# Kernel tuning notes

Measured on AMD Instinct MI355X. Metric: run time of the kernel, lower is better.

The kernel has to match this reference:

```python
import jax, jax.numpy as jnp
import numpy as np

DIM = 512
MAX_LEN = 2048
SHARED = 128
EXPAND = 2 * DIM  # expansion_factor * dim
PROJ = 2 * EXPAND + SHARED
EPS = 1e-6
BATCH = 8


def _rope(x):
    # x: [n, d]; rotates last dim (split-half RoPE) with position along axis 0
    n, d = x.shape
    half = d // 2
    freq = jnp.arange(half, dtype=x.dtype) / float(half)
    inv_freq = 10000.0 ** (-freq)
    sinusoid = jnp.arange(n, dtype=x.dtype)[:, None] * inv_freq[None, :]  # [n, half]
    sin, cos = jnp.sin(sinusoid), jnp.cos(sinusoid)
    x1, x2 = x[:, :half], x[:, half:]
    return jnp.concatenate([x1 * cos - x2 * sin, x2 * cos + x1 * sin], axis=-1)


def _toeplitz_rope(n, a, b):
    # a, b: [max_len]; tile to [n, max_len], rope over positions, then outer product
    ar = _rope(jnp.tile(a[None, :], (n, 1)))
    br = _rope(jnp.tile(b[None, :], (n, 1)))
    return jnp.einsum('mk,nk->mn', ar, br)  # [n, n]


def setup_inputs() -> dict:
    key = jax.random.key(0)
    ks = jax.random.split(key, 8)
    std = 0.02
    return {
        'x': jax.random.normal(ks[0], (BATCH, MAX_LEN, DIM), jnp.float32),
        'W1': std * jax.random.normal(ks[1], (DIM, PROJ), jnp.float32),
        'b1': jnp.zeros((PROJ,), jnp.float32),
        'W2': std * jax.random.normal(ks[2], (EXPAND, DIM), jnp.float32),
        'b2': jnp.zeros((DIM,), jnp.float32),
        'rope_a': std * jax.random.normal(ks[3], (MAX_LEN,), jnp.float32),
        'rope_b': std * jax.random.normal(ks[4], (MAX_LEN,), jnp.float32),
        'gamma': std * jax.random.normal(ks[5], (2, SHARED), jnp.float32),
        'beta': jnp.zeros((2, SHARED), jnp.float32),
        'norm_scale': jnp.asarray(1.0, jnp.float32),
    }


def reference(x, W1, b1, W2, b2, rope_a, rope_b, gamma, beta, norm_scale):
    shortcut = x
    # ScaledNorm: x * rsqrt(mean(x^2)) * scale
    ms = jnp.mean(jnp.square(x), axis=-1, keepdims=True)
    xn = x * jax.lax.rsqrt(ms + EPS) * norm_scale
    # proj1 with swish activation
    uv = jax.nn.swish(xn @ W1 + b1)  # [b, n, PROJ]
    u = uv[..., :EXPAND]
    v = uv[..., EXPAND:2 * EXPAND]
    base = uv[..., 2 * EXPAND:]  # [b, n, SHARED]
    qk_base = base[:, :, None, :] * gamma + beta  # [b, n, 2, SHARED]
    q, k = qk_base[:, :, 0, :], qk_base[:, :, 1, :]
    qk = jnp.einsum('bnd,bmd->bnm', q, k) / float(MAX_LEN)
    qk = qk + _toeplitz_rope(MAX_LEN, rope_a, rope_b)
    kernel = jnp.square(jax.nn.relu(qk))  # sqrrelu
    o = u * jnp.einsum('bnm,bme->bne', kernel, v)
    return o @ W2 + b2 + shortcut
```

## Files before the change

kernel.cpp:

```cpp
#include <hip/hip_runtime.h>
#include <math.h>

#define SEQ    2048
#define DIMM   512
#define SH     128
#define EXP    1024
#define PROJ_  2176
#define NBATCH 8
#define ROWS   16384

#define KER_SCALE     16384.0f
#define KER_SCALE_INV (1.0f / 16384.0f)
#define QK_INV        (1.0f / (4096.0f * 2048.0f))
#define W8            64.0f
#define INV4096       (1.0f / 4096.0f)

typedef __attribute__((ext_vector_type(4))) float floatx4;
typedef __attribute__((ext_vector_type(8))) int   int8v;

__device__ __forceinline__ unsigned short f2bf(float f) {
  union { float f; unsigned int u; } v; v.f = f;
  unsigned int r = (v.u + 0x7fffu + ((v.u >> 16) & 1u)) >> 16;
  return (unsigned short)r;
}
__device__ __forceinline__ float bf2f(unsigned short h) {
  union { unsigned int u; float f; } v; v.u = ((unsigned int)h) << 16;
  return v.f;
}
__device__ __forceinline__ unsigned char f2fp8(float f) {
  return (unsigned char)(__builtin_amdgcn_cvt_pk_fp8_f32(f, 0.0f, 0, false) & 0xffu);
}
__device__ __forceinline__ unsigned int pk4fp8(float a, float b, float c, float d) {
  unsigned int w = __builtin_amdgcn_cvt_pk_fp8_f32(a, b, 0, false);
  return __builtin_amdgcn_cvt_pk_fp8_f32(c, d, w, true);
}
__device__ __forceinline__ float fp82f(unsigned char b) {
  int e = (b >> 3) & 15, m = b & 7;
  float v = ldexpf((float)(e ? (8 + m) : m), (e ? e : 1) - 10);
  return (b & 0x80) ? -v : v;
}

__device__ __forceinline__ void async16(const void* g, void* l) {
  __builtin_amdgcn_global_load_lds(
      (const __attribute__((address_space(1))) void*)g,
      (__attribute__((address_space(3))) void*)l, 16, 0, 0);
}

__device__ __forceinline__ void transpose_tile_fp8(const float* __restrict__ in,
                                                   unsigned char* __restrict__ out,
                                                   int R, int C, int bx, int by, float* tile) {
  int tx = threadIdx.x & 31, ty = threadIdx.x >> 5;
  int c0 = bx * 32, r0 = by * 32;
  #pragma unroll
  for (int j = 0; j < 32; j += 8)
    tile[(ty + j) * 33 + tx] = in[(long)(r0 + ty + j) * C + c0 + tx];
  __syncthreads();
  #pragma unroll
  for (int j = 0; j < 32; j += 8)
    out[(long)(c0 + ty + j) * R + r0 + tx] = f2fp8(tile[tx * 33 + ty + j] * W8);
}

__global__ void prep_kernel(const float* __restrict__ x, const float* __restrict__ ns,
                            unsigned char* __restrict__ xq,
                            const float* __restrict__ W1, unsigned char* __restrict__ w1q,
                            const float* __restrict__ W2, unsigned char* __restrict__ w2q,
                            const float* __restrict__ ra, const float* __restrict__ rb,
                            float* __restrict__ tpl) {
  __shared__ float sh[33 * 32];
  const int b = blockIdx.x, tid = threadIdx.x;
  if (b < 4096) {
    int wave = tid >> 6, lane = tid & 63;
    long row = (long)b * 4 + wave;
    const float4* xr = (const float4*)(x + row * DIMM);
    float4 v0 = xr[lane], v1 = xr[lane + 64];
    float ss = v0.x*v0.x + v0.y*v0.y + v0.z*v0.z + v0.w*v0.w
             + v1.x*v1.x + v1.y*v1.y + v1.z*v1.z + v1.w*v1.w;
    #pragma unroll
    for (int o = 32; o > 0; o >>= 1) ss += __shfl_xor(ss, o);
    float sc = rsqrtf(ss * (1.0f / DIMM) + 1e-6f) * ns[0] * W8;
    uint2 pk;
    pk.x = pk4fp8(v0.x*sc, v0.y*sc, v0.z*sc, v0.w*sc);
    pk.y = pk4fp8(v1.x*sc, v1.y*sc, v1.z*sc, v1.w*sc);
    ((uint2*)(xq + row * DIMM))[lane] = pk;
  } else if (b < 4096 + 4095) {
    const int d = (b - 4096) - 2047;
    float sum = 0.0f;
    for (int k = tid; k < 1024; k += 256) {
      float a1 = ra[k], a2 = ra[k + 1024];
      float b1v = rb[k], b2v = rb[k + 1024];
      float p = a1 * b1v + a2 * b2v;
      float q = a1 * b2v - a2 * b1v;
      float th = exp2f((float)k * (-13.287712379549449f / 1024.0f));
      float ang = (float)d * th;
      sum += p * cosf(ang) + q * sinf(ang);
    }
    #pragma unroll
    for (int o = 32; o > 0; o >>= 1) sum += __shfl_xor(sum, o);
    int wave = tid >> 6, lane = tid & 63;
    if (lane == 0) sh[wave] = sum;
    __syncthreads();
    if (tid == 0) tpl[b - 4096] = sh[0] + sh[1] + sh[2] + sh[3];
  } else if (b < 9279) {
    int t = b - 8191;
    transpose_tile_fp8(W1, w1q, DIMM, PROJ_, t % 68, t / 68, sh);
  } else {
    int t = b - 9279;
    transpose_tile_fp8(W2, w2q, EXP, DIMM, t % 16, t / 16, sh);
  }
}

__device__ __forceinline__ void mfma_core_mx(const unsigned char* __restrict__ A,
                                             const unsigned char* __restrict__ B,
                                             int K, long rowBase, long colBase,
                                             unsigned char* smem, floatx4 acc[4][4]) {
  unsigned char* As = smem;
  unsigned char* Bs = smem + 128 * 128;
  const int tid  = threadIdx.x;
  const int wave = tid >> 6;
  const int lane = tid & 63;
  const int wr   = (wave >> 1) * 64;
  const int wc   = (wave & 1) * 64;
  const int r_l  = lane >> 3;
  const int c8   = lane & 7;
  const int fm   = lane & 15;
  const int fq   = lane >> 4;

  floatx4 z = {0.0f, 0.0f, 0.0f, 0.0f};
  #pragma unroll
  for (int mi = 0; mi < 4; ++mi)
    #pragma unroll
    for (int ni = 0; ni < 4; ++ni) acc[mi][ni] = z;

  union U8 { uint4 q[2]; int8v v; };

  for (int k0 = 0; k0 < K; k0 += 128) {
    __syncthreads();
    #pragma unroll
    for (int j = 0; j < 4; ++j) {
      int row = j * 32 + wave * 8 + r_l;
      int g = c8 ^ (row & 7);
      async16(A + (rowBase + row) * (long)K + k0 + g * 16, As + (j * 32 + wave * 8) * 128);
      async16(B + (colBase + row) * (long)K + k0 + g * 16, Bs + (j * 32 + wave * 8) * 128);
    }
    __syncthreads();
    int8v av[4], bv[4];
    #pragma unroll
    for (int mi = 0; mi < 4; ++mi) {
      int row = wr + mi * 16 + fm;
      int s0 = (2 * fq) ^ (row & 7);
      U8 u;
      u.q[0] = *(const uint4*)(As + row * 128 + s0 * 16);
      u.q[1] = *(const uint4*)(As + row * 128 + (s0 ^ 1) * 16);
      av[mi] = u.v;
    }
    #pragma unroll
    for (int ni = 0; ni < 4; ++ni) {
      int row = wc + ni * 16 + fm;
      int s0 = (2 * fq) ^ (row & 7);
      U8 u;
      u.q[0] = *(const uint4*)(Bs + row * 128 + s0 * 16);
      u.q[1] = *(const uint4*)(Bs + row * 128 + (s0 ^ 1) * 16);
      bv[ni] = u.v;
    }
    #pragma unroll
    for (int mi = 0; mi < 4; ++mi)
      #pragma unroll
      for (int ni = 0; ni < 4; ++ni)
        acc[mi][ni] = __builtin_amdgcn_mfma_scale_f32_16x16x128_f8f6f4(
            av[mi], bv[ni], acc[mi][ni], 0, 0, 0, 0x7F7F7F7F, 0, 0x7F7F7F7F);
  }
}

#define EPILOGUE_VARS                                         \
  const int lane = threadIdx.x & 63, wave = threadIdx.x >> 6; \
  const int wr = (wave >> 1) * 64, wc = (wave & 1) * 64;      \
  const int fr = (lane >> 4) * 4, fc = lane & 15;

__global__ void __launch_bounds__(256)
gemm_uv(const unsigned char* __restrict__ xq,
        const unsigned char* __restrict__ w1q,
        const float* __restrict__ b1,
        const float* __restrict__ gamma,
        const float* __restrict__ beta,
        unsigned char* __restrict__ uq,
        unsigned char* __restrict__ vT,
        unsigned char* __restrict__ qq,
        unsigned char* __restrict__ kq) {
  __shared__ __align__(16) unsigned short smem[17408];
  floatx4 acc[4][4];
  long rowBase = (long)blockIdx.x * 128;
  long colBase = (long)blockIdx.y * 128;
  mfma_core_mx(xq, w1q, DIMM, rowBase, colBase, (unsigned char*)smem, acc);
  EPILOGUE_VARS

  if (blockIdx.y < 8) {
    #pragma unroll
    for (int mi = 0; mi < 4; ++mi)
    #pragma unroll
    for (int ni = 0; ni < 4; ++ni)
    #pragma unroll
    for (int i = 0; i < 4; ++i) {
      long row = rowBase + wr + mi * 16 + fr + i;
      long col = colBase + wc + ni * 16 + fc;
      float t = acc[mi][ni][i] * INV4096 + b1[col];
      uq[row * EXP + col] = f2fp8(t / (1.0f + __expf(-t)) * W8);
    }
  } else if (blockIdx.y < 16) {
    __syncthreads();
    #pragma unroll
    for (int mi = 0; mi < 4; ++mi)
    #pragma unroll
    for (int ni = 0; ni < 4; ++ni)
    #pragma unroll
    for (int i = 0; i < 4; ++i) {
      int rl = wr + mi * 16 + fr + i;
      int cl = wc + ni * 16 + fc;
      long col = colBase + cl;
      float t = acc[mi][ni][i] * INV4096 + b1[col];
      smem[cl * 136 + rl] = f2bf(t / (1.0f + __expf(-t)));
    }
    __syncthreads();
    long b_   = rowBase >> 11;
    long nblk = rowBase & 2047;
    long e0   = colBase - EXP;
    #pragma unroll
    for (int rep = 0; rep < 8; ++rep) {
      int cl = rep * 16 + (threadIdx.x >> 4);
      int n0 = (threadIdx.x & 15) * 8;
      const unsigned short* src = smem + cl * 136 + n0;
      uint2 pk;
      pk.x = pk4fp8(bf2f(src[0]), bf2f(src[1]), bf2f(src[2]), bf2f(src[3]));
      pk.y = pk4fp8(bf2f(src[4]), bf2f(src[5]), bf2f(src[6]), bf2f(src[7]));
      *(uint2*)(vT + (b_ * EXP + e0 + cl) * (long)SEQ + nblk + n0) = pk;
    }
  } else {
    #pragma unroll
    for (int mi = 0; mi < 4; ++mi)
    #pragma unroll
    for (int ni = 0; ni < 4; ++ni)
    #pragma unroll
    for (int i = 0; i < 4; ++i) {
      long row = rowBase + wr + mi * 16 + fr + i;
      long col = colBase + wc + ni * 16 + fc;
      float t = acc[mi][ni][i] * INV4096 + b1[col];
      float s = t / (1.0f + __expf(-t));
      int dd = (int)(col - 2 * EXP);
      qq[row * SH + dd] = f2fp8((s * gamma[dd] + beta[dd]) * W8);
      kq[row * SH + dd] = f2fp8((s * gamma[SH + dd] + beta[SH + dd]) * W8);
    }
  }
}

__global__ void __launch_bounds__(256)
gemm_qk(const unsigned char* __restrict__ kq,
        const unsigned char* __restrict__ qq,
        const float* __restrict__ tpl,
        unsigned char* __restrict__ ker) {
  __shared__ __align__(16) unsigned char smem8[32768];
  floatx4 acc[4][4];
  int L = blockIdx.x;
  long b = L & 7;
  int w = L >> 3;
  long mBase = (long)(w & 15) * 128;
  long nBase = (long)(w >> 4) * 128;
  mfma_core_mx(kq + b * SEQ * SH, qq + b * SEQ * SH, SH, mBase, nBase, smem8, acc);
  unsigned char* kerb = ker + b * (long)SEQ * SEQ;
  EPILOGUE_VARS
  (void)fr;
  __syncthreads();
  #pragma unroll
  for (int mi = 0; mi < 4; ++mi)
  #pragma unroll
  for (int ni = 0; ni < 4; ++ni) {
    int m_loc0 = wr + mi * 16 + (lane >> 4) * 4;
    int n_loc  = wc + ni * 16 + fc;
    long n = nBase + n_loc;
    long m0 = mBase + m_loc0;
    float v[4];
    #pragma unroll
    for (int i = 0; i < 4; ++i) {
      float val = acc[mi][ni][i] * QK_INV + tpl[n - (m0 + i) + 2047];
      float r = fmaxf(val, 0.0f);
      v[i] = fminf(r * r * KER_SCALE, 440.0f);
    }
    *(unsigned int*)(smem8 + n_loc * 136 + m_loc0) = pk4fp8(v[0], v[1], v[2], v[3]);
  }
  __syncthreads();
  #pragma unroll
  for (int rep = 0; rep < 4; ++rep) {
    int n_loc = rep * 32 + (threadIdx.x >> 3);
    int m_seg = (threadIdx.x & 7) * 16;
    uint4 v16 = *(const uint4*)(smem8 + n_loc * 136 + m_seg);
    *(uint4*)(kerb + (nBase + n_loc) * (long)SEQ + mBase + m_seg) = v16;
  }
}

__global__ void __launch_bounds__(256)
gemm_pv(const unsigned char* __restrict__ ker,
        const unsigned char* __restrict__ vT,
        const unsigned char* __restrict__ uq,
        unsigned char* __restrict__ obq) {
  __shared__ __align__(16) unsigned char smem8[32768];
  floatx4 acc[4][4];
  int L = blockIdx.x;
  long b = L & 7;
  int w = L >> 3;
  long eBase = (long)(w & 7) * 128;
  long nBase = (long)(w >> 3) * 128;
  mfma_core_mx(vT + b * (long)EXP * SEQ, ker + b * (long)SEQ * SEQ, SEQ,
               eBase, nBase, smem8, acc);
  const unsigned char* ub = uq + b * (long)SEQ * EXP;
  unsigned char* obb = obq + b * (long)SEQ * EXP;
  EPILOGUE_VARS
  (void)fr;
  __syncthreads();
  #pragma unroll
  for (int mi = 0; mi < 4; ++mi)
  #pragma unroll
  for (int ni = 0; ni < 4; ++ni) {
    int e_loc0 = wr + mi * 16 + (lane >> 4) * 4;
    int n_loc  = wc + ni * 16 + fc;
    unsigned int uw = *(const unsigned int*)(ub + (nBase + n_loc) * (long)EXP + eBase + e_loc0);
    float v[4];
    #pragma unroll
    for (int i = 0; i < 4; ++i) {
      float u = fp82f((unsigned char)(uw >> (8 * i)));
      v[i] = acc[mi][ni][i] * KER_SCALE_INV * u;
    }
    *(unsigned int*)(smem8 + n_loc * 136 + e_loc0) = pk4fp8(v[0], v[1], v[2], v[3]);
  }
  __syncthreads();
  #pragma unroll
  for (int rep = 0; rep < 4; ++rep) {
    int n_loc = rep * 32 + (threadIdx.x >> 3);
    int e_seg = (threadIdx.x & 7) * 16;
    uint4 v16 = *(const uint4*)(smem8 + n_loc * 136 + e_seg);
    *(uint4*)(obb + (nBase + n_loc) * (long)EXP + eBase + e_seg) = v16;
  }
}

__global__ void __launch_bounds__(256)
gemm_out(const unsigned char* __restrict__ obq,
         const unsigned char* __restrict__ w2q,
         const float* __restrict__ b2,
         const float* __restrict__ x,
         float* __restrict__ out) {
  __shared__ __align__(16) unsigned char smem8[32768];
  floatx4 acc[4][4];
  long rowBase = (long)blockIdx.x * 128;
  long colBase = (long)blockIdx.y * 128;
  mfma_core_mx(obq, w2q, EXP, rowBase, colBase, smem8, acc);
  EPILOGUE_VARS
  #pragma unroll
  for (int mi = 0; mi < 4; ++mi)
  #pragma unroll
  for (int ni = 0; ni < 4; ++ni)
  #pragma unroll
  for (int i = 0; i < 4; ++i) {
    long row = rowBase + wr + mi * 16 + fr + i;
    long col = colBase + wc + ni * 16 + fc;
    out[row * DIMM + col] = acc[mi][ni][i] * INV4096 + b2[col] + x[row * DIMM + col];
  }
}

extern "C" void kernel_launch(void* const* d_in, const int* in_sizes, int n_in,
                              void* d_out, int out_size, void* d_ws, size_t ws_size,
                              hipStream_t stream) {
  const float* x          = (const float*)d_in[0];
  const float* W1         = (const float*)d_in[1];
  const float* b1         = (const float*)d_in[2];
  const float* W2         = (const float*)d_in[3];
  const float* b2         = (const float*)d_in[4];
  const float* rope_a     = (const float*)d_in[5];
  const float* rope_b     = (const float*)d_in[6];
  const float* gamma      = (const float*)d_in[7];
  const float* beta       = (const float*)d_in[8];
  const float* norm_scale = (const float*)d_in[9];
  float* out = (float*)d_out;

  char* ws = (char*)d_ws;
  size_t off = 0;
  auto nxt = [&](size_t bytes) -> void* {
    void* p = ws + off;
    off += (bytes + 255) & ~(size_t)255;
    return p;
  };
  unsigned char*  xq  = (unsigned char*)nxt((size_t)ROWS * DIMM);
  unsigned char*  w1q = (unsigned char*)nxt((size_t)PROJ_ * DIMM);
  unsigned char*  w2q = (unsigned char*)nxt((size_t)DIMM * EXP);
  unsigned char*  uq  = (unsigned char*)nxt((size_t)ROWS * EXP);
  unsigned char*  vT  = (unsigned char*)nxt((size_t)NBATCH * EXP * SEQ);
  unsigned char*  qq  = (unsigned char*)nxt((size_t)ROWS * SH);
  unsigned char*  kq  = (unsigned char*)nxt((size_t)ROWS * SH);
  float*          tpl = (float*)nxt((size_t)4096 * 4);
  unsigned char*  ker = (unsigned char*)nxt((size_t)NBATCH * SEQ * SEQ);
  unsigned char*  obq = (unsigned char*)nxt((size_t)ROWS * EXP);

  prep_kernel<<<9791, 256, 0, stream>>>(x, norm_scale, xq, W1, w1q, W2, w2q,
                                        rope_a, rope_b, tpl);
  gemm_uv<<<dim3(ROWS / 128, PROJ_ / 128), 256, 0, stream>>>(xq, w1q, b1, gamma, beta,
                                                             uq, vT, qq, kq);
  gemm_qk<<<2048, 256, 0, stream>>>(kq, qq, tpl, ker);
  gemm_pv<<<1024, 256, 0, stream>>>(ker, vT, uq, obq);
  gemm_out<<<dim3(ROWS / 128, DIMM / 128), 256, 0, stream>>>(obq, w2q, b2, x, out);
}
```

Measured before the change: 225.3 us.

## Double-buffer LDS tiles in MX-FP8 GEMM core with async prefetch

Rewrites the shared GEMM mainloop to use two LDS buffers, prefetching the next K-tile with async loads while MFMAs run on the current one. This replaces the two barriers per iteration with one and hoists the address arithmetic out of the loop. It also raises wave priority around the MFMA block. LDS per block doubles to 64KB, which may reduce occupancy.

Result: no change. 223.8 us (-0.7%).

```diff
diff --git a/kernel.cpp b/kernel.cpp
--- a/kernel.cpp
+++ b/kernel.cpp
@@ -113,8 +113,6 @@
                                              const unsigned char* __restrict__ B,
                                              int K, long rowBase, long colBase,
                                              unsigned char* smem, floatx4 acc[4][4]) {
-  unsigned char* As = smem;
-  unsigned char* Bs = smem + 128 * 128;
   const int tid  = threadIdx.x;
   const int wave = tid >> 6;
   const int lane = tid & 63;
@@ -131,18 +129,41 @@
     #pragma unroll
     for (int ni = 0; ni < 4; ++ni) acc[mi][ni] = z;
 
+  const unsigned char* aSrc[4];
+  const unsigned char* bSrc[4];
+  int ldsOff[4];
+  #pragma unroll
+  for (int j = 0; j < 4; ++j) {
+    int row = j * 32 + wave * 8 + r_l;
+    int g = c8 ^ (row & 7);
+    aSrc[j] = A + (rowBase + row) * (long)K + g * 16;
+    bSrc[j] = B + (colBase + row) * (long)K + g * 16;
+    ldsOff[j] = (j * 32 + wave * 8) * 128;
+  }
+
   union U8 { uint4 q[2]; int8v v; };
-
-  for (int k0 = 0; k0 < K; k0 += 128) {
-    __syncthreads();
-    #pragma unroll
-    for (int j = 0; j < 4; ++j) {
-      int row = j * 32 + wave * 8 + r_l;
-      int g = c8 ^ (row & 7);
-      async16(A + (rowBase + row) * (long)K + k0 + g * 16, As + (j * 32 + wave * 8) * 128);
-      async16(B + (colBase + row) * (long)K + k0 + g * 16, Bs + (j * 32 + wave * 8) * 128);
-    }
-    __syncthreads();
+  const int nt = K >> 7;
+
+  #pragma unroll
+  for (int j = 0; j < 4; ++j) {
+    async16(aSrc[j], smem + ldsOff[j]);
+    async16(bSrc[j], smem + 16384 + ldsOff[j]);
+  }
+  __syncthreads();
+
+  int cur = 0;
+  for (int t = 0; t < nt; ++t) {
+    unsigned char* As = smem + cur * 32768;
+    unsigned char* Bs = As + 16384;
+    if (t + 1 < nt) {
+      unsigned char* An = smem + (cur ^ 1) * 32768;
+      int k0 = (t + 1) << 7;
+      #pragma unroll
+      for (int j = 0; j < 4; ++j) {
+        async16(aSrc[j] + k0, An + ldsOff[j]);
+        async16(bSrc[j] + k0, An + 16384 + ldsOff[j]);
+      }
+    }
     int8v av[4], bv[4];
     #pragma unroll
     for (int mi = 0; mi < 4; ++mi) {
@@ -162,12 +183,16 @@
       u.q[1] = *(const uint4*)(Bs + row * 128 + (s0 ^ 1) * 16);
       bv[ni] = u.v;
     }
+    __builtin_amdgcn_s_setprio(1);
     #pragma unroll
     for (int mi = 0; mi < 4; ++mi)
       #pragma unroll
       for (int ni = 0; ni < 4; ++ni)
         acc[mi][ni] = __builtin_amdgcn_mfma_scale_f32_16x16x128_f8f6f4(
             av[mi], bv[ni], acc[mi][ni], 0, 0, 0, 0x7F7F7F7F, 0, 0x7F7F7F7F);
+    __builtin_amdgcn_s_setprio(0);
+    __syncthreads();
+    cur ^= 1;
   }
 }
 
@@ -186,11 +211,12 @@
         unsigned char* __restrict__ vT,
         unsigned char* __restrict__ qq,
         unsigned char* __restrict__ kq) {
-  __shared__ __align__(16) unsigned short smem[17408];
+  __shared__ __align__(16) unsigned char smem8[65536];
+  unsigned short* smem = (unsigned short*)smem8;
   floatx4 acc[4][4];
   long rowBase = (long)blockIdx.x * 128;
   long colBase = (long)blockIdx.y * 128;
-  mfma_core_mx(xq, w1q, DIMM, rowBase, colBase, (unsigned char*)smem, acc);
+  mfma_core_mx(xq, w1q, DIMM, rowBase, colBase, smem8, acc);
   EPILOGUE_VARS
 
   if (blockIdx.y < 8) {
@@ -256,7 +282,7 @@
         const unsigned char* __restrict__ qq,
         const float* __restrict__ tpl,
         unsigned char* __restrict__ ker) {
-  __shared__ __align__(16) unsigned char smem8[32768];
+  __shared__ __align__(16) unsigned char smem8[65536];
   floatx4 acc[4][4];
   int L = blockIdx.x;
   long b = L & 7;
@@ -300,7 +326,7 @@
         const unsigned char* __restrict__ vT,
         const unsigned char* __restrict__ uq,
         unsigned char* __restrict__ obq) {
-  __shared__ __align__(16) unsigned char smem8[32768];
+  __shared__ __align__(16) unsigned char smem8[65536];
   floatx4 acc[4][4];
   int L = blockIdx.x;
   long b = L & 7;
@@ -345,7 +371,7 @@
          const float* __restrict__ b2,
          const float* __restrict__ x,
          float* __restrict__ out) {
-  __shared__ __align__(16) unsigned char smem8[32768];
+  __shared__ __align__(16) unsigned char smem8[65536];
   floatx4 acc[4][4];
   long rowBase = (long)blockIdx.x * 128;
   long colBase = (long)blockIdx.y * 128;
```
